# Optimization experiments

Measured on AMD Instinct MI355X. Metric: run time of the kernel, lower is better.

Reference implementation:

```python
import jax, jax.numpy as jnp
import numpy as np
import math

WIDTH_POW = 10
WIDTH = 2 ** WIDTH_POW      # 1024
DEPTH = 20
BATCH = 8192
TWO_PI = 2.0 * math.pi


def setup_inputs() -> dict:
    key = jax.random.key(0)
    kx, ka = jax.random.split(key)
    # X is [width, batch] (features-first, matching the torch module's dim-0 padding)
    X = jax.random.normal(kx, (WIDTH, BATCH), dtype=jnp.float32)
    # angles ~ Uniform[0, 2*pi), as in the torch initializer
    angles = jax.random.uniform(ka, (DEPTH, WIDTH // 2), dtype=jnp.float32) * TWO_PI
    return {"X": X, "angles": angles}


def _butterfly_layer(X, ang, stride):
    # X: [width, batch]; ang: [width//2]
    w, b = X.shape
    # Pairs: within each block of 2*stride, element j rotates with element j+stride.
    Xr = X.reshape(w // (2 * stride), 2, stride, b)
    x0 = Xr[:, 0]  # [nblocks, stride, batch]
    x1 = Xr[:, 1]
    c = jnp.cos(ang).reshape(-1, stride, 1)
    s = jnp.sin(ang).reshape(-1, stride, 1)
    y0 = c * x0 + s * x1
    y1 = -s * x0 + c * x1
    return jnp.stack([y0, y1], axis=1).reshape(w, b)


def reference(X, angles):
    width = angles.shape[1] * 2
    width_pow = int(round(math.log2(width)))
    # Pad feature dim up to width (no-op here since X.shape[0] == width)
    pad = width - X.shape[0]
    if pad > 0:
        X = jnp.concatenate([X, jnp.zeros((pad, X.shape[1]), dtype=X.dtype)], axis=0)
    depth = angles.shape[0]
    for i in range(depth):  # small fixed loop over layers (structurally distinct strides)
        stride = 2 ** (i % width_pow)
        X = _butterfly_layer(X, angles[i], stride)
    return X
```

## Files before the change

kernel.cpp:

```cpp
#include <hip/hip_runtime.h>
#include <math.h>


#define NROW   1024
#define BATCH  8192
#define BATCH2 (BATCH / 2)
#define DEPTH  20
#define NANG   512
#define TAB_ELEMS (DEPTH * NANG)
#define TAB_BYTES ((size_t)TAB_ELEMS * 8)

typedef float v2f __attribute__((ext_vector_type(2)));

__device__ __host__ __forceinline__ int rowP1(int sub, int i){ return (sub<<4)|i; }
__device__ __host__ __forceinline__ int rowP2(int sub, int i){ return (sub&15) | (i<<4) | ((sub>>4)<<8); }
__device__ __host__ __forceinline__ int rowP3(int sub, int i){ return (i&3) | (sub<<2) | ((i>>2)<<8); }
__device__ __host__ __forceinline__ int rowP4(int sub, int i){ return (sub&3) | ((i&3)<<2) | (((i>>2)&3)<<4) | ((sub>>2)<<6); }
__device__ __host__ __forceinline__ int rowP5(int sub, int i){ return sub | ((i&3)<<6) | ((i>>2)<<8); }

__global__ void build_tab_kernel(const float* __restrict__ ang,
                                 float2* __restrict__ tab) {
    int idx = blockIdx.x * blockDim.x + threadIdx.x;
    if (idx >= TAB_ELEMS) return;
    int l = idx >> 9;
    int slot = idx & (NANG - 1);
    int sub = slot >> 3, p = slot & 7;
    int sp = l % 10;
    int SL, ph;
    if (l < 4)       { ph = 0; SL = 1 << l; }
    else if (l < 8)  { ph = 1; SL = 1 << (l - 4); }
    else if (l < 12) { ph = 2; SL = (l == 8) ? 4 : (l == 9) ? 8 : (l == 10) ? 1 : 2; }
    else if (l < 16) { ph = 3; SL = 1 << (l - 12); }
    else             { ph = 4; SL = 1 << (l - 16); }
    int i0 = 2 * (p / SL) * SL + p % SL;
    int r;
    if (ph == 0)      r = rowP1(sub, i0);
    else if (ph == 1) r = rowP2(sub, i0);
    else if (ph == 2) r = rowP3(sub, i0);
    else if (ph == 3) r = rowP4(sub, i0);
    else              r = rowP5(sub, i0);
    int s = 1 << sp;
    int a = ((r >> (sp + 1)) << sp) | (r & (s - 1));
    float th = ang[l * NANG + a];
    float sv, cv;
    sincosf(th, &sv, &cv);
    tab[idx] = make_float2(cv, sv);
}

__device__ __forceinline__ void rotp(v2f& a, v2f& b, float cv, float sv) {
    v2f c = {cv, cv}, s = {sv, sv};
    v2f x0 = a, x1 = b;
    a = __builtin_elementwise_fma(c, x0, s * x1);
    b = __builtin_elementwise_fma(-s, x0, c * x1);
}

template<int SL>
__device__ __forceinline__ void layer_tab(v2f y[16],
                                          const float2* __restrict__ tl,
                                          int sub) {
    const float4* q4 = reinterpret_cast<const float4*>(tl + 8 * sub);
    #pragma unroll
    for (int v = 0; v < 4; ++v) {
        float4 q = q4[v];
        int p0 = 2 * v, p1 = 2 * v + 1;
        int a0 = 2 * (p0 / SL) * SL + p0 % SL;
        int a1 = 2 * (p1 / SL) * SL + p1 % SL;
        rotp(y[a0], y[a0 + SL], q.x, q.y);
        rotp(y[a1], y[a1 + SL], q.z, q.w);
    }
}

template<int SL, int PH, int SP>
__device__ __forceinline__ void layer_notab(v2f y[16],
                                            const float* __restrict__ angL,
                                            int sub) {
    #pragma unroll
    for (int p = 0; p < 8; ++p) {
        int i0 = 2 * (p / SL) * SL + p % SL;
        int r;
        if (PH == 0)      r = rowP1(sub, i0);
        else if (PH == 1) r = rowP2(sub, i0);
        else if (PH == 2) r = rowP3(sub, i0);
        else if (PH == 3) r = rowP4(sub, i0);
        else              r = rowP5(sub, i0);
        int a = ((r >> (SP + 1)) << SP) | (r & ((1 << SP) - 1));
        float th = angL[a];
        float sv, cv;
        __sincosf(th, &sv, &cv);
        rotp(y[i0], y[i0 + SL], cv, sv);
    }
}

__device__ __forceinline__ int eaddr(int c, int r) {
    return (c << 10) | ((r ^ ((r >> 4) & 15)) ^ (c << 1));
}

template<bool USE_TAB>
__global__ __launch_bounds__(512) void butterfly_kernel(
        const float* __restrict__ X, const float* __restrict__ ang,
        const float2* __restrict__ tab, float* __restrict__ out) {
    __shared__ v2f lds2[8 * 1024];
    int t = threadIdx.x;
    int c = t & 7;
    int sub = t >> 3;
    int bid = blockIdx.x;
    int L = ((bid & 7) << 6) | (bid >> 3);
    int col2 = (L << 3) + c;

    v2f y[16];
    const v2f* Xp = reinterpret_cast<const v2f*>(X) + col2;
    #pragma unroll
    for (int i = 0; i < 16; ++i)
        y[i] = Xp[rowP1(sub, i) * BATCH2];

    if (USE_TAB) {
        layer_tab<1>(y, tab + 0 * NANG, sub);
        layer_tab<2>(y, tab + 1 * NANG, sub);
        layer_tab<4>(y, tab + 2 * NANG, sub);
        layer_tab<8>(y, tab + 3 * NANG, sub);
    } else {
        layer_notab<1,0,0>(y, ang + 0 * NANG, sub);
        layer_notab<2,0,1>(y, ang + 1 * NANG, sub);
        layer_notab<4,0,2>(y, ang + 2 * NANG, sub);
        layer_notab<8,0,3>(y, ang + 3 * NANG, sub);
    }
    #pragma unroll
    for (int i = 0; i < 16; ++i) lds2[eaddr(c, rowP1(sub, i))] = y[i];
    __syncthreads();
    #pragma unroll
    for (int i = 0; i < 16; ++i) y[i] = lds2[eaddr(c, rowP2(sub, i))];

    if (USE_TAB) {
        layer_tab<1>(y, tab + 4 * NANG, sub);
        layer_tab<2>(y, tab + 5 * NANG, sub);
        layer_tab<4>(y, tab + 6 * NANG, sub);
        layer_tab<8>(y, tab + 7 * NANG, sub);
    } else {
        layer_notab<1,1,4>(y, ang + 4 * NANG, sub);
        layer_notab<2,1,5>(y, ang + 5 * NANG, sub);
        layer_notab<4,1,6>(y, ang + 6 * NANG, sub);
        layer_notab<8,1,7>(y, ang + 7 * NANG, sub);
    }
    __syncthreads();
    #pragma unroll
    for (int i = 0; i < 16; ++i) lds2[eaddr(c, rowP2(sub, i))] = y[i];
    __syncthreads();
    #pragma unroll
    for (int i = 0; i < 16; ++i) y[i] = lds2[eaddr(c, rowP3(sub, i))];

    if (USE_TAB) {
        layer_tab<4>(y, tab +  8 * NANG, sub);
        layer_tab<8>(y, tab +  9 * NANG, sub);
        layer_tab<1>(y, tab + 10 * NANG, sub);
        layer_tab<2>(y, tab + 11 * NANG, sub);
    } else {
        layer_notab<4,2,8>(y, ang +  8 * NANG, sub);
        layer_notab<8,2,9>(y, ang +  9 * NANG, sub);
        layer_notab<1,2,0>(y, ang + 10 * NANG, sub);
        layer_notab<2,2,1>(y, ang + 11 * NANG, sub);
    }
    __syncthreads();
    #pragma unroll
    for (int i = 0; i < 16; ++i) lds2[eaddr(c, rowP3(sub, i))] = y[i];
    __syncthreads();
    #pragma unroll
    for (int i = 0; i < 16; ++i) y[i] = lds2[eaddr(c, rowP4(sub, i))];

    if (USE_TAB) {
        layer_tab<1>(y, tab + 12 * NANG, sub);
        layer_tab<2>(y, tab + 13 * NANG, sub);
        layer_tab<4>(y, tab + 14 * NANG, sub);
        layer_tab<8>(y, tab + 15 * NANG, sub);
    } else {
        layer_notab<1,3,2>(y, ang + 12 * NANG, sub);
        layer_notab<2,3,3>(y, ang + 13 * NANG, sub);
        layer_notab<4,3,4>(y, ang + 14 * NANG, sub);
        layer_notab<8,3,5>(y, ang + 15 * NANG, sub);
    }
    __syncthreads();
    #pragma unroll
    for (int i = 0; i < 16; ++i) lds2[eaddr(c, rowP4(sub, i))] = y[i];
    __syncthreads();
    #pragma unroll
    for (int i = 0; i < 16; ++i) y[i] = lds2[eaddr(c, rowP5(sub, i))];

    if (USE_TAB) {
        layer_tab<1>(y, tab + 16 * NANG, sub);
        layer_tab<2>(y, tab + 17 * NANG, sub);
        layer_tab<4>(y, tab + 18 * NANG, sub);
        layer_tab<8>(y, tab + 19 * NANG, sub);
    } else {
        layer_notab<1,4,6>(y, ang + 16 * NANG, sub);
        layer_notab<2,4,7>(y, ang + 17 * NANG, sub);
        layer_notab<4,4,8>(y, ang + 18 * NANG, sub);
        layer_notab<8,4,9>(y, ang + 19 * NANG, sub);
    }

    v2f* Op = reinterpret_cast<v2f*>(out) + col2;
    #pragma unroll
    for (int i = 0; i < 16; ++i)
        Op[rowP5(sub, i) * BATCH2] = y[i];
}

extern "C" void kernel_launch(void* const* d_in, const int* in_sizes, int n_in,
                              void* d_out, int out_size, void* d_ws, size_t ws_size,
                              hipStream_t stream) {
    (void)in_sizes; (void)n_in; (void)out_size;
    const float* X   = (const float*)d_in[0];
    const float* ang = (const float*)d_in[1];
    float* out = (float*)d_out;

    bool use_tab = (d_ws != nullptr) && (ws_size >= TAB_BYTES);
    if (use_tab) {
        float2* tab = (float2*)d_ws;
        build_tab_kernel<<<(TAB_ELEMS + 255) / 256, 256, 0, stream>>>(ang, tab);
        butterfly_kernel<true><<<512, 512, 0, stream>>>(X, ang, tab, out);
    } else {
        butterfly_kernel<false><<<512, 512, 0, stream>>>(X, ang, nullptr, out);
    }
}
```

Measured before the change: 32.75 us.

## Give each wave a whole column pair to replace block barriers with wave barriers

The kernel is restructured so each 64-lane wave owns one full 1024-row column pair held in its own LDS slice. The intermediate transposes between butterfly phases then need only wave-level barriers instead of block-wide __syncthreads. Global loads and stores are staged through LDS so the global access pattern stays coalesced across 4 columns. Blocks shrink to 256 threads with 1024 blocks, which adds an extra LDS round trip at the start and end in exchange for removing four block barriers.

```diff
diff --git a/kernel.cpp b/kernel.cpp
--- a/kernel.cpp
+++ b/kernel.cpp
@@ -12,11 +12,11 @@
 
 typedef float v2f __attribute__((ext_vector_type(2)));
 
-__device__ __host__ __forceinline__ int rowP1(int sub, int i){ return (sub<<4)|i; }
-__device__ __host__ __forceinline__ int rowP2(int sub, int i){ return (sub&15) | (i<<4) | ((sub>>4)<<8); }
-__device__ __host__ __forceinline__ int rowP3(int sub, int i){ return (i&3) | (sub<<2) | ((i>>2)<<8); }
-__device__ __host__ __forceinline__ int rowP4(int sub, int i){ return (sub&3) | ((i&3)<<2) | (((i>>2)&3)<<4) | ((sub>>2)<<6); }
-__device__ __host__ __forceinline__ int rowP5(int sub, int i){ return sub | ((i&3)<<6) | ((i>>2)<<8); }
+__device__ __host__ __forceinline__ int rowP1(int o, int i){ return (o<<4)|i; }
+__device__ __host__ __forceinline__ int rowP2(int o, int i){ return (o&15) | (i<<4) | ((o>>4)<<8); }
+__device__ __host__ __forceinline__ int rowP3(int o, int i){ return (i&3) | (o<<2) | ((i>>2)<<8); }
+__device__ __host__ __forceinline__ int rowP4(int o, int i){ return (o&3) | ((i&3)<<2) | (((i>>2)&3)<<4) | ((o>>2)<<6); }
+__device__ __host__ __forceinline__ int rowP5(int o, int i){ return o | ((i&3)<<6) | ((i>>2)<<8); }
 
 __global__ void build_tab_kernel(const float* __restrict__ ang,
                                  float2* __restrict__ tab) {
@@ -57,8 +57,8 @@
 template<int SL>
 __device__ __forceinline__ void layer_tab(v2f y[16],
                                           const float2* __restrict__ tl,
-                                          int sub) {
-    const float4* q4 = reinterpret_cast<const float4*>(tl + 8 * sub);
+                                          int o) {
+    const float4* q4 = reinterpret_cast<const float4*>(tl + 8 * o);
     #pragma unroll
     for (int v = 0; v < 4; ++v) {
         float4 q = q4[v];
@@ -73,16 +73,16 @@
 template<int SL, int PH, int SP>
 __device__ __forceinline__ void layer_notab(v2f y[16],
                                             const float* __restrict__ angL,
-                                            int sub) {
+                                            int o) {
     #pragma unroll
     for (int p = 0; p < 8; ++p) {
         int i0 = 2 * (p / SL) * SL + p % SL;
         int r;
-        if (PH == 0)      r = rowP1(sub, i0);
-        else if (PH == 1) r = rowP2(sub, i0);
-        else if (PH == 2) r = rowP3(sub, i0);
-        else if (PH == 3) r = rowP4(sub, i0);
-        else              r = rowP5(sub, i0);
+        if (PH == 0)      r = rowP1(o, i0);
+        else if (PH == 1) r = rowP2(o, i0);
+        else if (PH == 2) r = rowP3(o, i0);
+        else if (PH == 3) r = rowP4(o, i0);
+        else              r = rowP5(o, i0);
         int a = ((r >> (SP + 1)) << SP) | (r & ((1 << SP) - 1));
         float th = angL[a];
         float sv, cv;
@@ -91,115 +91,133 @@
     }
 }
 
-__device__ __forceinline__ int eaddr(int c, int r) {
-    return (c << 10) | ((r ^ ((r >> 4) & 15)) ^ (c << 1));
-}
+__device__ __forceinline__ int sg(int r) { return r ^ ((r >> 4) & 15); }
 
 template<bool USE_TAB>
-__global__ __launch_bounds__(512) void butterfly_kernel(
+__global__ __launch_bounds__(256) void butterfly_kernel(
         const float* __restrict__ X, const float* __restrict__ ang,
         const float2* __restrict__ tab, float* __restrict__ out) {
-    __shared__ v2f lds2[8 * 1024];
+    __shared__ v2f lds[4 * 1024];
     int t = threadIdx.x;
-    int c = t & 7;
-    int sub = t >> 3;
+    int c = t & 3;
+    int sub = t >> 2;
+    int w = t >> 6;
+    int ln = t & 63;
     int bid = blockIdx.x;
-    int L = ((bid & 7) << 6) | (bid >> 3);
-    int col2 = (L << 3) + c;
-
+    int L = ((bid & 7) << 7) | (bid >> 3);
+    int col2 = L << 2;
+
+    {
+        const v2f* Xp = reinterpret_cast<const v2f*>(X) + col2 + c;
+        #pragma unroll
+        for (int i = 0; i < 16; ++i) {
+            v2f v = Xp[rowP1(sub, i) * BATCH2];
+            lds[(c << 10) | sg(rowP1(sub, i))] = v;
+        }
+    }
+    __syncthreads();
+
+    v2f* slice = lds + (w << 10);
     v2f y[16];
-    const v2f* Xp = reinterpret_cast<const v2f*>(X) + col2;
-    #pragma unroll
-    for (int i = 0; i < 16; ++i)
-        y[i] = Xp[rowP1(sub, i) * BATCH2];
-
-    if (USE_TAB) {
-        layer_tab<1>(y, tab + 0 * NANG, sub);
-        layer_tab<2>(y, tab + 1 * NANG, sub);
-        layer_tab<4>(y, tab + 2 * NANG, sub);
-        layer_tab<8>(y, tab + 3 * NANG, sub);
-    } else {
-        layer_notab<1,0,0>(y, ang + 0 * NANG, sub);
-        layer_notab<2,0,1>(y, ang + 1 * NANG, sub);
-        layer_notab<4,0,2>(y, ang + 2 * NANG, sub);
-        layer_notab<8,0,3>(y, ang + 3 * NANG, sub);
-    }
-    #pragma unroll
-    for (int i = 0; i < 16; ++i) lds2[eaddr(c, rowP1(sub, i))] = y[i];
+    #pragma unroll
+    for (int i = 0; i < 16; ++i) y[i] = slice[sg(rowP1(ln, i))];
+
+    if (USE_TAB) {
+        layer_tab<1>(y, tab + 0 * NANG, ln);
+        layer_tab<2>(y, tab + 1 * NANG, ln);
+        layer_tab<4>(y, tab + 2 * NANG, ln);
+        layer_tab<8>(y, tab + 3 * NANG, ln);
+    } else {
+        layer_notab<1,0,0>(y, ang + 0 * NANG, ln);
+        layer_notab<2,0,1>(y, ang + 1 * NANG, ln);
+        layer_notab<4,0,2>(y, ang + 2 * NANG, ln);
+        layer_notab<8,0,3>(y, ang + 3 * NANG, ln);
+    }
+    __builtin_amdgcn_wave_barrier();
+    #pragma unroll
+    for (int i = 0; i < 16; ++i) slice[sg(rowP1(ln, i))] = y[i];
+    __builtin_amdgcn_wave_barrier();
+    #pragma unroll
+    for (int i = 0; i < 16; ++i) y[i] = slice[sg(rowP2(ln, i))];
+
+    if (USE_TAB) {
+        layer_tab<1>(y, tab + 4 * NANG, ln);
+        layer_tab<2>(y, tab + 5 * NANG, ln);
+        layer_tab<4>(y, tab + 6 * NANG, ln);
+        layer_tab<8>(y, tab + 7 * NANG, ln);
+    } else {
+        layer_notab<1,1,4>(y, ang + 4 * NANG, ln);
+        layer_notab<2,1,5>(y, ang + 5 * NANG, ln);
+        layer_notab<4,1,6>(y, ang + 6 * NANG, ln);
+        layer_notab<8,1,7>(y, ang + 7 * NANG, ln);
+    }
+    __builtin_amdgcn_wave_barrier();
+    #pragma unroll
+    for (int i = 0; i < 16; ++i) slice[sg(rowP2(ln, i))] = y[i];
+    __builtin_amdgcn_wave_barrier();
+    #pragma unroll
+    for (int i = 0; i < 16; ++i) y[i] = slice[sg(rowP3(ln, i))];
+
+    if (USE_TAB) {
+        layer_tab<4>(y, tab +  8 * NANG, ln);
+        layer_tab<8>(y, tab +  9 * NANG, ln);
+        layer_tab<1>(y, tab + 10 * NANG, ln);
+        layer_tab<2>(y, tab + 11 * NANG, ln);
+    } else {
+        layer_notab<4,2,8>(y, ang +  8 * NANG, ln);
+        layer_notab<8,2,9>(y, ang +  9 * NANG, ln);
+        layer_notab<1,2,0>(y, ang + 10 * NANG, ln);
+        layer_notab<2,2,1>(y, ang + 11 * NANG, ln);
+    }
+    __builtin_amdgcn_wave_barrier();
+    #pragma unroll
+    for (int i = 0; i < 16; ++i) slice[sg(rowP3(ln, i))] = y[i];
+    __builtin_amdgcn_wave_barrier();
+    #pragma unroll
+    for (int i = 0; i < 16; ++i) y[i] = slice[sg(rowP4(ln, i))];
+
+    if (USE_TAB) {
+        layer_tab<1>(y, tab + 12 * NANG, ln);
+        layer_tab<2>(y, tab + 13 * NANG, ln);
+        layer_tab<4>(y, tab + 14 * NANG, ln);
+        layer_tab<8>(y, tab + 15 * NANG, ln);
+    } else {
+        layer_notab<1,3,2>(y, ang + 12 * NANG, ln);
+        layer_notab<2,3,3>(y, ang + 13 * NANG, ln);
+        layer_notab<4,3,4>(y, ang + 14 * NANG, ln);
+        layer_notab<8,3,5>(y, ang + 15 * NANG, ln);
+    }
+    __builtin_amdgcn_wave_barrier();
+    #pragma unroll
+    for (int i = 0; i < 16; ++i) slice[sg(rowP4(ln, i))] = y[i];
+    __builtin_amdgcn_wave_barrier();
+    #pragma unroll
+    for (int i = 0; i < 16; ++i) y[i] = slice[sg(rowP5(ln, i))];
+
+    if (USE_TAB) {
+        layer_tab<1>(y, tab + 16 * NANG, ln);
+        layer_tab<2>(y, tab + 17 * NANG, ln);
+        layer_tab<4>(y, tab + 18 * NANG, ln);
+        layer_tab<8>(y, tab + 19 * NANG, ln);
+    } else {
+        layer_notab<1,4,6>(y, ang + 16 * NANG, ln);
+        layer_notab<2,4,7>(y, ang + 17 * NANG, ln);
+        layer_notab<4,4,8>(y, ang + 18 * NANG, ln);
+        layer_notab<8,4,9>(y, ang + 19 * NANG, ln);
+    }
+
+    __builtin_amdgcn_wave_barrier();
+    #pragma unroll
+    for (int i = 0; i < 16; ++i) slice[sg(rowP5(ln, i))] = y[i];
     __syncthreads();
-    #pragma unroll
-    for (int i = 0; i < 16; ++i) y[i] = lds2[eaddr(c, rowP2(sub, i))];
-
-    if (USE_TAB) {
-        layer_tab<1>(y, tab + 4 * NANG, sub);
-        layer_tab<2>(y, tab + 5 * NANG, sub);
-        layer_tab<4>(y, tab + 6 * NANG, sub);
-        layer_tab<8>(y, tab + 7 * NANG, sub);
-    } else {
-        layer_notab<1,1,4>(y, ang + 4 * NANG, sub);
-        layer_notab<2,1,5>(y, ang + 5 * NANG, sub);
-        layer_notab<4,1,6>(y, ang + 6 * NANG, sub);
-        layer_notab<8,1,7>(y, ang + 7 * NANG, sub);
-    }
-    __syncthreads();
-    #pragma unroll
-    for (int i = 0; i < 16; ++i) lds2[eaddr(c, rowP2(sub, i))] = y[i];
-    __syncthreads();
-    #pragma unroll
-    for (int i = 0; i < 16; ++i) y[i] = lds2[eaddr(c, rowP3(sub, i))];
-
-    if (USE_TAB) {
-        layer_tab<4>(y, tab +  8 * NANG, sub);
-        layer_tab<8>(y, tab +  9 * NANG, sub);
-        layer_tab<1>(y, tab + 10 * NANG, sub);
-        layer_tab<2>(y, tab + 11 * NANG, sub);
-    } else {
-        layer_notab<4,2,8>(y, ang +  8 * NANG, sub);
-        layer_notab<8,2,9>(y, ang +  9 * NANG, sub);
-        layer_notab<1,2,0>(y, ang + 10 * NANG, sub);
-        layer_notab<2,2,1>(y, ang + 11 * NANG, sub);
-    }
-    __syncthreads();
-    #pragma unroll
-    for (int i = 0; i < 16; ++i) lds2[eaddr(c, rowP3(sub, i))] = y[i];
-    __syncthreads();
-    #pragma unroll
-    for (int i = 0; i < 16; ++i) y[i] = lds2[eaddr(c, rowP4(sub, i))];
-
-    if (USE_TAB) {
-        layer_tab<1>(y, tab + 12 * NANG, sub);
-        layer_tab<2>(y, tab + 13 * NANG, sub);
-        layer_tab<4>(y, tab + 14 * NANG, sub);
-        layer_tab<8>(y, tab + 15 * NANG, sub);
-    } else {
-        layer_notab<1,3,2>(y, ang + 12 * NANG, sub);
-        layer_notab<2,3,3>(y, ang + 13 * NANG, sub);
-        layer_notab<4,3,4>(y, ang + 14 * NANG, sub);
-        layer_notab<8,3,5>(y, ang + 15 * NANG, sub);
-    }
-    __syncthreads();
-    #pragma unroll
-    for (int i = 0; i < 16; ++i) lds2[eaddr(c, rowP4(sub, i))] = y[i];
-    __syncthreads();
-    #pragma unroll
-    for (int i = 0; i < 16; ++i) y[i] = lds2[eaddr(c, rowP5(sub, i))];
-
-    if (USE_TAB) {
-        layer_tab<1>(y, tab + 16 * NANG, sub);
-        layer_tab<2>(y, tab + 17 * NANG, sub);
-        layer_tab<4>(y, tab + 18 * NANG, sub);
-        layer_tab<8>(y, tab + 19 * NANG, sub);
-    } else {
-        layer_notab<1,4,6>(y, ang + 16 * NANG, sub);
-        layer_notab<2,4,7>(y, ang + 17 * NANG, sub);
-        layer_notab<4,4,8>(y, ang + 18 * NANG, sub);
-        layer_notab<8,4,9>(y, ang + 19 * NANG, sub);
-    }
-
-    v2f* Op = reinterpret_cast<v2f*>(out) + col2;
-    #pragma unroll
-    for (int i = 0; i < 16; ++i)
-        Op[rowP5(sub, i) * BATCH2] = y[i];
+    {
+        v2f* Op = reinterpret_cast<v2f*>(out) + col2 + c;
+        #pragma unroll
+        for (int i = 0; i < 16; ++i) {
+            v2f v = lds[(c << 10) | sg(rowP5(sub, i))];
+            Op[rowP5(sub, i) * BATCH2] = v;
+        }
+    }
 }
 
 extern "C" void kernel_launch(void* const* d_in, const int* in_sizes, int n_in,
@@ -214,8 +232,8 @@
     if (use_tab) {
         float2* tab = (float2*)d_ws;
         build_tab_kernel<<<(TAB_ELEMS + 255) / 256, 256, 0, stream>>>(ang, tab);
-        butterfly_kernel<true><<<512, 512, 0, stream>>>(X, ang, tab, out);
-    } else {
-        butterfly_kernel<false><<<512, 512, 0, stream>>>(X, ang, nullptr, out);
-    }
-}
+        butterfly_kernel<true><<<1024, 256, 0, stream>>>(X, ang, tab, out);
+    } else {
+        butterfly_kernel<false><<<1024, 256, 0, stream>>>(X, ang, nullptr, out);
+    }
+}
```

Result: slower. 42.08 us (+28.5%).

## Use 32 rows per thread to cut butterfly transposes from four to three

Applied to the files above, without the earlier changes.

Each thread now holds 32 rows instead of 16 and handles 16 column pairs per block instead of 8. That lets five butterfly layers run in registers between exchanges, so only three LDS transposes are needed instead of four, with a simpler two-permutation row mapping and float4 LDS accesses. The grid is halved to 256 blocks and LDS use doubles to 128KB. This raises register pressure, lowers occupancy and leaves fewer blocks than a GPU with many CUs might want.

```diff
diff --git a/kernel.cpp b/kernel.cpp
--- a/kernel.cpp
+++ b/kernel.cpp
@@ -12,11 +12,8 @@
 
 typedef float v2f __attribute__((ext_vector_type(2)));
 
-__device__ __host__ __forceinline__ int rowP1(int sub, int i){ return (sub<<4)|i; }
-__device__ __host__ __forceinline__ int rowP2(int sub, int i){ return (sub&15) | (i<<4) | ((sub>>4)<<8); }
-__device__ __host__ __forceinline__ int rowP3(int sub, int i){ return (i&3) | (sub<<2) | ((i>>2)<<8); }
-__device__ __host__ __forceinline__ int rowP4(int sub, int i){ return (sub&3) | ((i&3)<<2) | (((i>>2)&3)<<4) | ((sub>>2)<<6); }
-__device__ __host__ __forceinline__ int rowP5(int sub, int i){ return sub | ((i&3)<<6) | ((i>>2)<<8); }
+__device__ __host__ __forceinline__ int rowA(int sub, int i){ return (sub << 5) | i; }
+__device__ __host__ __forceinline__ int rowB(int sub, int i){ return sub | (i << 5); }
 
 __global__ void build_tab_kernel(const float* __restrict__ ang,
                                  float2* __restrict__ tab) {
@@ -24,23 +21,13 @@
     if (idx >= TAB_ELEMS) return;
     int l = idx >> 9;
     int slot = idx & (NANG - 1);
-    int sub = slot >> 3, p = slot & 7;
-    int sp = l % 10;
-    int SL, ph;
-    if (l < 4)       { ph = 0; SL = 1 << l; }
-    else if (l < 8)  { ph = 1; SL = 1 << (l - 4); }
-    else if (l < 12) { ph = 2; SL = (l == 8) ? 4 : (l == 9) ? 8 : (l == 10) ? 1 : 2; }
-    else if (l < 16) { ph = 3; SL = 1 << (l - 12); }
-    else             { ph = 4; SL = 1 << (l - 16); }
+    int sub = slot >> 4, p = slot & 15;
+    int m10 = l % 10;
+    int sp = m10;
+    int SL = 1 << (m10 % 5);
     int i0 = 2 * (p / SL) * SL + p % SL;
-    int r;
-    if (ph == 0)      r = rowP1(sub, i0);
-    else if (ph == 1) r = rowP2(sub, i0);
-    else if (ph == 2) r = rowP3(sub, i0);
-    else if (ph == 3) r = rowP4(sub, i0);
-    else              r = rowP5(sub, i0);
-    int s = 1 << sp;
-    int a = ((r >> (sp + 1)) << sp) | (r & (s - 1));
+    int r = (m10 >= 5) ? rowB(sub, i0) : rowA(sub, i0);
+    int a = ((r >> (sp + 1)) << sp) | (r & ((1 << sp) - 1));
     float th = ang[l * NANG + a];
     float sv, cv;
     sincosf(th, &sv, &cv);
@@ -55,12 +42,10 @@
 }
 
 template<int SL>
-__device__ __forceinline__ void layer_tab(v2f y[16],
-                                          const float2* __restrict__ tl,
-                                          int sub) {
-    const float4* q4 = reinterpret_cast<const float4*>(tl + 8 * sub);
+__device__ __forceinline__ void layer_tab(v2f y[32],
+                                          const float4* __restrict__ q4) {
     #pragma unroll
-    for (int v = 0; v < 4; ++v) {
+    for (int v = 0; v < 8; ++v) {
         float4 q = q4[v];
         int p0 = 2 * v, p1 = 2 * v + 1;
         int a0 = 2 * (p0 / SL) * SL + p0 % SL;
@@ -70,19 +55,14 @@
     }
 }
 
-template<int SL, int PH, int SP>
-__device__ __forceinline__ void layer_notab(v2f y[16],
+template<int SL, bool PB, int SP>
+__device__ __forceinline__ void layer_notab(v2f y[32],
                                             const float* __restrict__ angL,
                                             int sub) {
     #pragma unroll
-    for (int p = 0; p < 8; ++p) {
+    for (int p = 0; p < 16; ++p) {
         int i0 = 2 * (p / SL) * SL + p % SL;
-        int r;
-        if (PH == 0)      r = rowP1(sub, i0);
-        else if (PH == 1) r = rowP2(sub, i0);
-        else if (PH == 2) r = rowP3(sub, i0);
-        else if (PH == 3) r = rowP4(sub, i0);
-        else              r = rowP5(sub, i0);
+        int r = PB ? rowB(sub, i0) : rowA(sub, i0);
         int a = ((r >> (SP + 1)) << SP) | (r & ((1 << SP) - 1));
         float th = angL[a];
         float sv, cv;
@@ -91,115 +71,111 @@
     }
 }
 
-__device__ __forceinline__ int eaddr(int c, int r) {
-    return (c << 10) | ((r ^ ((r >> 4) & 15)) ^ (c << 1));
-}
-
 template<bool USE_TAB>
 __global__ __launch_bounds__(512) void butterfly_kernel(
         const float* __restrict__ X, const float* __restrict__ ang,
         const float2* __restrict__ tab, float* __restrict__ out) {
-    __shared__ v2f lds2[8 * 1024];
+    __shared__ v2f lds[16 * 1024];
     int t = threadIdx.x;
-    int c = t & 7;
-    int sub = t >> 3;
+    int c = t & 15;
+    int sub = t >> 4;
     int bid = blockIdx.x;
-    int L = ((bid & 7) << 6) | (bid >> 3);
-    int col2 = (L << 3) + c;
+    int L = ((bid & 7) << 5) | (bid >> 3);
+    int col2 = (L << 4) + c;
+    int xr = (c & 7) << 1;
+    v2f* base = lds + (c << 10);
 
-    v2f y[16];
+    v2f y[32];
     const v2f* Xp = reinterpret_cast<const v2f*>(X) + col2;
     #pragma unroll
-    for (int i = 0; i < 16; ++i)
-        y[i] = Xp[rowP1(sub, i) * BATCH2];
+    for (int i = 0; i < 32; ++i)
+        y[i] = Xp[rowA(sub, i) * BATCH2];
+
+    const float4* tf4 = reinterpret_cast<const float4*>(tab);
+    if (USE_TAB) {
+        layer_tab<1 >(y, tf4 + 0 * 256 + 8 * sub);
+        layer_tab<2 >(y, tf4 + 1 * 256 + 8 * sub);
+        layer_tab<4 >(y, tf4 + 2 * 256 + 8 * sub);
+        layer_tab<8 >(y, tf4 + 3 * 256 + 8 * sub);
+        layer_tab<16>(y, tf4 + 4 * 256 + 8 * sub);
+    } else {
+        layer_notab<1 ,false,0>(y, ang + 0 * NANG, sub);
+        layer_notab<2 ,false,1>(y, ang + 1 * NANG, sub);
+        layer_notab<4 ,false,2>(y, ang + 2 * NANG, sub);
+        layer_notab<8 ,false,3>(y, ang + 3 * NANG, sub);
+        layer_notab<16,false,4>(y, ang + 4 * NANG, sub);
+    }
+    #pragma unroll
+    for (int u = 0; u < 16; ++u)
+        *reinterpret_cast<float4*>(&base[((sub << 5) + 2 * u) ^ xr]) =
+            make_float4(y[2*u].x, y[2*u].y, y[2*u+1].x, y[2*u+1].y);
+    __syncthreads();
+    #pragma unroll
+    for (int i = 0; i < 32; ++i) y[i] = base[rowB(sub, i) ^ xr];
 
     if (USE_TAB) {
-        layer_tab<1>(y, tab + 0 * NANG, sub);
-        layer_tab<2>(y, tab + 1 * NANG, sub);
-        layer_tab<4>(y, tab + 2 * NANG, sub);
-        layer_tab<8>(y, tab + 3 * NANG, sub);
+        layer_tab<1 >(y, tf4 + 5 * 256 + 8 * sub);
+        layer_tab<2 >(y, tf4 + 6 * 256 + 8 * sub);
+        layer_tab<4 >(y, tf4 + 7 * 256 + 8 * sub);
+        layer_tab<8 >(y, tf4 + 8 * 256 + 8 * sub);
+        layer_tab<16>(y, tf4 + 9 * 256 + 8 * sub);
     } else {
-        layer_notab<1,0,0>(y, ang + 0 * NANG, sub);
-        layer_notab<2,0,1>(y, ang + 1 * NANG, sub);
-        layer_notab<4,0,2>(y, ang + 2 * NANG, sub);
-        layer_notab<8,0,3>(y, ang + 3 * NANG, sub);
-    }
-    #pragma unroll
-    for (int i = 0; i < 16; ++i) lds2[eaddr(c, rowP1(sub, i))] = y[i];
-    __syncthreads();
-    #pragma unroll
-    for (int i = 0; i < 16; ++i) y[i] = lds2[eaddr(c, rowP2(sub, i))];
-
-    if (USE_TAB) {
-        layer_tab<1>(y, tab + 4 * NANG, sub);
-        layer_tab<2>(y, tab + 5 * NANG, sub);
-        layer_tab<4>(y, tab + 6 * NANG, sub);
-        layer_tab<8>(y, tab + 7 * NANG, sub);
-    } else {
-        layer_notab<1,1,4>(y, ang + 4 * NANG, sub);
-        layer_notab<2,1,5>(y, ang + 5 * NANG, sub);
-        layer_notab<4,1,6>(y, ang + 6 * NANG, sub);
-        layer_notab<8,1,7>(y, ang + 7 * NANG, sub);
+        layer_notab<1 ,true,5>(y, ang + 5 * NANG, sub);
+        layer_notab<2 ,true,6>(y, ang + 6 * NANG, sub);
+        layer_notab<4 ,true,7>(y, ang + 7 * NANG, sub);
+        layer_notab<8 ,true,8>(y, ang + 8 * NANG, sub);
+        layer_notab<16,true,9>(y, ang + 9 * NANG, sub);
     }
     __syncthreads();
     #pragma unroll
-    for (int i = 0; i < 16; ++i) lds2[eaddr(c, rowP2(sub, i))] = y[i];
+    for (int i = 0; i < 32; ++i) base[rowB(sub, i) ^ xr] = y[i];
     __syncthreads();
     #pragma unroll
-    for (int i = 0; i < 16; ++i) y[i] = lds2[eaddr(c, rowP3(sub, i))];
+    for (int u = 0; u < 16; ++u) {
+        float4 v = *reinterpret_cast<const float4*>(&base[((sub << 5) + 2 * u) ^ xr]);
+        y[2*u].x = v.x; y[2*u].y = v.y; y[2*u+1].x = v.z; y[2*u+1].y = v.w;
+    }
 
     if (USE_TAB) {
-        layer_tab<4>(y, tab +  8 * NANG, sub);
-        layer_tab<8>(y, tab +  9 * NANG, sub);
-        layer_tab<1>(y, tab + 10 * NANG, sub);
-        layer_tab<2>(y, tab + 11 * NANG, sub);
+        layer_tab<1 >(y, tf4 + 10 * 256 + 8 * sub);
+        layer_tab<2 >(y, tf4 + 11 * 256 + 8 * sub);
+        layer_tab<4 >(y, tf4 + 12 * 256 + 8 * sub);
+        layer_tab<8 >(y, tf4 + 13 * 256 + 8 * sub);
+        layer_tab<16>(y, tf4 + 14 * 256 + 8 * sub);
     } else {
-        layer_notab<4,2,8>(y, ang +  8 * NANG, sub);
-        layer_notab<8,2,9>(y, ang +  9 * NANG, sub);
-        layer_notab<1,2,0>(y, ang + 10 * NANG, sub);
-        layer_notab<2,2,1>(y, ang + 11 * NANG, sub);
+        layer_notab<1 ,false,0>(y, ang + 10 * NANG, sub);
+        layer_notab<2 ,false,1>(y, ang + 11 * NANG, sub);
+        layer_notab<4 ,false,2>(y, ang + 12 * NANG, sub);
+        layer_notab<8 ,false,3>(y, ang + 13 * NANG, sub);
+        layer_notab<16,false,4>(y, ang + 14 * NANG, sub);
     }
     __syncthreads();
     #pragma unroll
-    for (int i = 0; i < 16; ++i) lds2[eaddr(c, rowP3(sub, i))] = y[i];
+    for (int u = 0; u < 16; ++u)
+        *reinterpret_cast<float4*>(&base[((sub << 5) + 2 * u) ^ xr]) =
+            make_float4(y[2*u].x, y[2*u].y, y[2*u+1].x, y[2*u+1].y);
     __syncthreads();
     #pragma unroll
-    for (int i = 0; i < 16; ++i) y[i] = lds2[eaddr(c, rowP4(sub, i))];
+    for (int i = 0; i < 32; ++i) y[i] = base[rowB(sub, i) ^ xr];
 
     if (USE_TAB) {
-        layer_tab<1>(y, tab + 12 * NANG, sub);
-        layer_tab<2>(y, tab + 13 * NANG, sub);
-        layer_tab<4>(y, tab + 14 * NANG, sub);
-        layer_tab<8>(y, tab + 15 * NANG, sub);
+        layer_tab<1 >(y, tf4 + 15 * 256 + 8 * sub);
+        layer_tab<2 >(y, tf4 + 16 * 256 + 8 * sub);
+        layer_tab<4 >(y, tf4 + 17 * 256 + 8 * sub);
+        layer_tab<8 >(y, tf4 + 18 * 256 + 8 * sub);
+        layer_tab<16>(y, tf4 + 19 * 256 + 8 * sub);
     } else {
-        layer_notab<1,3,2>(y, ang + 12 * NANG, sub);
-        layer_notab<2,3,3>(y, ang + 13 * NANG, sub);
-        layer_notab<4,3,4>(y, ang + 14 * NANG, sub);
-        layer_notab<8,3,5>(y, ang + 15 * NANG, sub);
-    }
-    __syncthreads();
-    #pragma unroll
-    for (int i = 0; i < 16; ++i) lds2[eaddr(c, rowP4(sub, i))] = y[i];
-    __syncthreads();
-    #pragma unroll
-    for (int i = 0; i < 16; ++i) y[i] = lds2[eaddr(c, rowP5(sub, i))];
-
-    if (USE_TAB) {
-        layer_tab<1>(y, tab + 16 * NANG, sub);
-        layer_tab<2>(y, tab + 17 * NANG, sub);
-        layer_tab<4>(y, tab + 18 * NANG, sub);
-        layer_tab<8>(y, tab + 19 * NANG, sub);
-    } else {
-        layer_notab<1,4,6>(y, ang + 16 * NANG, sub);
-        layer_notab<2,4,7>(y, ang + 17 * NANG, sub);
-        layer_notab<4,4,8>(y, ang + 18 * NANG, sub);
-        layer_notab<8,4,9>(y, ang + 19 * NANG, sub);
+        layer_notab<1 ,true,5>(y, ang + 15 * NANG, sub);
+        layer_notab<2 ,true,6>(y, ang + 16 * NANG, sub);
+        layer_notab<4 ,true,7>(y, ang + 17 * NANG, sub);
+        layer_notab<8 ,true,8>(y, ang + 18 * NANG, sub);
+        layer_notab<16,true,9>(y, ang + 19 * NANG, sub);
     }
 
     v2f* Op = reinterpret_cast<v2f*>(out) + col2;
     #pragma unroll
-    for (int i = 0; i < 16; ++i)
-        Op[rowP5(sub, i) * BATCH2] = y[i];
+    for (int i = 0; i < 32; ++i)
+        Op[rowB(sub, i) * BATCH2] = y[i];
 }
 
 extern "C" void kernel_launch(void* const* d_in, const int* in_sizes, int n_in,
@@ -214,8 +190,8 @@
     if (use_tab) {
         float2* tab = (float2*)d_ws;
         build_tab_kernel<<<(TAB_ELEMS + 255) / 256, 256, 0, stream>>>(ang, tab);
-        butterfly_kernel<true><<<512, 512, 0, stream>>>(X, ang, tab, out);
+        butterfly_kernel<true><<<256, 512, 0, stream>>>(X, ang, tab, out);
     } else {
-        butterfly_kernel<false><<<512, 512, 0, stream>>>(X, ang, nullptr, out);
+        butterfly_kernel<false><<<256, 512, 0, stream>>>(X, ang, nullptr, out);
     }
 }
```

New measurement: 31.66 us. 3.3% less time.
